# Kernel optimization log

Measured on AMD Instinct MI355X. Metric: run time of the kernel, lower is better.

Reference implementation:

```python
import jax, jax.numpy as jnp
import numpy as np

N, B, T = 2048, 16, 256

def setup_inputs() -> dict:
    key = jax.random.key(0)
    k1, k2, k3, k4 = jax.random.split(key, 4)
    x = jax.random.normal(k1, (B, T, N), dtype=jnp.float32)
    weight = jax.random.normal(k2, (T, T), dtype=jnp.float32) * (1.0 / np.sqrt(T))
    bias = jax.random.normal(k3, (T,), dtype=jnp.float32) * 0.01
    # Gumbel(0,1) noise, matching torch.nn.functional.gumbel_softmax internals
    u = jax.random.uniform(k4, (N * N, 2), dtype=jnp.float32, minval=1e-6, maxval=1.0 - 1e-6)
    gumbel = -jnp.log(-jnp.log(u))
    return {"x": x, "weight": weight, "bias": bias, "gumbel": gumbel}

def reference(x, weight, bias, gumbel):
    # x: [B, T, N] -> node-major [N, B, T]
    xp = jnp.transpose(x, (2, 0, 1))
    n = xp.shape[0]
    # --- similarity-based logits (torch writes via .data -> no grad path) ---
    xs = jax.lax.stop_gradient(xp)
    x_avg = xs.mean(axis=1)                                          # [N, T]
    x_norm = x_avg / jnp.maximum(jnp.linalg.norm(x_avg, axis=-1, keepdims=True), 1e-12)
    sim = (x_norm @ x_norm.T + 1.0) * 0.5                            # [N, N] in [0,1]
    sim_flat = sim.reshape(-1)
    # gumbel_softmax(hard=True) forward: adjacency = argmax over (logits + g)
    score0 = sim_flat + gumbel[:, 0]
    score1 = (1.0 - sim_flat) + gumbel[:, 1]
    adj = (score0 > score1).astype(xp.dtype).reshape(n, n)           # directed adjacency
    # --- structural coefficient (dense, faithful to compute_structural_coeff) ---
    adj_sym = jnp.clip(adj + adj.T, 0.0, 1.0)
    nmask = jnp.clip(adj_sym + jnp.eye(n, dtype=xp.dtype), 0.0, 1.0)
    common = nmask @ nmask.T                                         # common-neighbor counts
    max_common = common.max()                                        # >= 1 (diagonal)
    valid = (adj_sym * (common > 1.0).astype(xp.dtype)) > 0
    struct = jnp.where(valid, (common / max_common) * common, 0.0)   # lambda_val = 1.0
    # edge weights only at directed-edge positions
    W = adj * struct                                                 # [src, dst]
    # --- gcn_norm (no self loops, improved=False): deg over dst, D^-1/2 W D^-1/2 ---
    deg = W.sum(axis=0)
    dinv = jnp.where(deg > 0, deg ** -0.5, 0.0)
    Wn = dinv[:, None] * W * dinv[None, :]
    # --- linear + gather-multiply-scatter aggregation (out[d] = sum_s Wn[s,d] x[s]) ---
    xw = jnp.einsum('nbt,to->nbo', xp, weight)                       # [N, B, T]
    out = jnp.einsum('sd,sbt->dbt', Wn, xw) + bias                   # [N, B, T]
    return jnp.transpose(out, (1, 2, 0))                             # [B, T, N]
```

## Files before the change

kernel.cpp:

```cpp
#include <hip/hip_runtime.h>

#define NN 2048
#define BB 16
#define TT 256

typedef unsigned short ushort_t;
typedef unsigned char u8;
typedef short bf16x8 __attribute__((ext_vector_type(8)));
typedef float f32x4 __attribute__((ext_vector_type(4)));
typedef int i32x4 __attribute__((ext_vector_type(4)));

__device__ __forceinline__ ushort_t f2bf(float f) {
    unsigned u = __float_as_uint(f);
    return (ushort_t)((u + 0x7FFFu + ((u >> 16) & 1u)) >> 16);
}

__device__ __forceinline__ void gload16(const void* g, void* l) {
    __builtin_amdgcn_global_load_lds((const __attribute__((address_space(1))) unsigned int*)g,
                                     (__attribute__((address_space(3))) unsigned int*)l,
                                     16, 0, 0);
}

__device__ __forceinline__ void loop_bf16_128x64(
    const ushort_t* __restrict__ Ag, size_t lda,
    const ushort_t* __restrict__ Bg, size_t ldb,
    int m0, int n0, int nkt,
    ushort_t (*As)[128][32], ushort_t (*Bs)[64][32],
    f32x4 (&acc)[4][2], int tid)
{
    const int lane = tid & 63, wave = tid >> 6;
    const int wr = wave >> 1, wc = wave & 1;
    const int r0 = tid >> 2, kc = (tid & 3) * 8;
    const int lr = lane & 15, kg = (lane >> 4) * 8;
    gload16(&Ag[(size_t)(m0 + r0) * lda + kc], &As[0][r0][kc]);
    gload16(&Ag[(size_t)(m0 + r0 + 64) * lda + kc], &As[0][r0 + 64][kc]);
    gload16(&Bg[(size_t)(n0 + r0) * ldb + kc], &Bs[0][r0][kc]);
    __syncthreads();
    int cur = 0;
    for (int kt = 0; kt < nkt; kt++) {
        if (kt + 1 < nkt) {
            const int k0 = (kt + 1) * 32;
            gload16(&Ag[(size_t)(m0 + r0) * lda + k0 + kc], &As[cur ^ 1][r0][kc]);
            gload16(&Ag[(size_t)(m0 + r0 + 64) * lda + k0 + kc], &As[cur ^ 1][r0 + 64][kc]);
            gload16(&Bg[(size_t)(n0 + r0) * ldb + k0 + kc], &Bs[cur ^ 1][r0][kc]);
        }
        bf16x8 af[4], bfj[2];
#pragma unroll
        for (int f = 0; f < 4; f++) af[f] = *(const bf16x8*)&As[cur][wr * 64 + f * 16 + lr][kg];
#pragma unroll
        for (int j = 0; j < 2; j++) bfj[j] = *(const bf16x8*)&Bs[cur][wc * 32 + j * 16 + lr][kg];
#pragma unroll
        for (int i = 0; i < 4; i++)
#pragma unroll
            for (int j = 0; j < 2; j++)
                acc[i][j] = __builtin_amdgcn_mfma_f32_16x16x32_bf16(af[i], bfj[j], acc[i][j], 0, 0, 0);
        __syncthreads();
        cur ^= 1;
    }
}

__device__ __forceinline__ void loop_i8_128x64(
    const u8* __restrict__ Ag, size_t lda,
    const u8* __restrict__ Bg, size_t ldb,
    int m0, int n0, int nkt,
    u8 (*As)[128][64], u8 (*Bs)[64][64],
    i32x4 (&acc)[4][2], int tid)
{
    const int lane = tid & 63, wave = tid >> 6;
    const int wr = wave >> 1, wc = wave & 1;
    const int r0 = tid >> 2, kc = (tid & 3) * 16;
    const int lr = lane & 15, kg = (lane >> 4) * 16;
    gload16(&Ag[(size_t)(m0 + r0) * lda + kc], &As[0][r0][kc]);
    gload16(&Ag[(size_t)(m0 + r0 + 64) * lda + kc], &As[0][r0 + 64][kc]);
    gload16(&Bg[(size_t)(n0 + r0) * ldb + kc], &Bs[0][r0][kc]);
    __syncthreads();
    int cur = 0;
    for (int kt = 0; kt < nkt; kt++) {
        if (kt + 1 < nkt) {
            const int k0 = (kt + 1) * 64;
            gload16(&Ag[(size_t)(m0 + r0) * lda + k0 + kc], &As[cur ^ 1][r0][kc]);
            gload16(&Ag[(size_t)(m0 + r0 + 64) * lda + k0 + kc], &As[cur ^ 1][r0 + 64][kc]);
            gload16(&Bg[(size_t)(n0 + r0) * ldb + k0 + kc], &Bs[cur ^ 1][r0][kc]);
        }
        i32x4 af[4], bfj[2];
#pragma unroll
        for (int f = 0; f < 4; f++) af[f] = *(const i32x4*)&As[cur][wr * 64 + f * 16 + lr][kg];
#pragma unroll
        for (int j = 0; j < 2; j++) bfj[j] = *(const i32x4*)&Bs[cur][wc * 32 + j * 16 + lr][kg];
#pragma unroll
        for (int i = 0; i < 4; i++)
#pragma unroll
            for (int j = 0; j < 2; j++)
                acc[i][j] = __builtin_amdgcn_mfma_i32_16x16x64_i8(af[i], bfj[j], acc[i][j], 0, 0, 0);
        __syncthreads();
        cur ^= 1;
    }
}

__global__ __launch_bounds__(256) void k_xts(const float* __restrict__ x,
                                             ushort_t* __restrict__ xT,
                                             float* __restrict__ xsumT,
                                             float* __restrict__ ssq) {
    __shared__ float tile[32][33];
    __shared__ float ssqp[32];
    const int n0 = blockIdx.x * 32, t0 = blockIdx.y * 32;
    const int tid = threadIdx.x;
    const int r = tid >> 3, c4 = (tid & 7) * 4;
    if (tid < 32) ssqp[tid] = 0.f;
    float4 acc = {0.f, 0.f, 0.f, 0.f};
    for (int b = 0; b < BB; b++) {
        const float4 v = *(const float4*)&x[(size_t)((b * TT) + t0 + r) * NN + n0 + c4];
        acc.x += v.x; acc.y += v.y; acc.z += v.z; acc.w += v.w;
        __syncthreads();
        tile[r][c4 + 0] = v.x; tile[r][c4 + 1] = v.y;
        tile[r][c4 + 2] = v.z; tile[r][c4 + 3] = v.w;
        __syncthreads();
        ushort4 o;
        o.x = f2bf(tile[c4 + 0][r]); o.y = f2bf(tile[c4 + 1][r]);
        o.z = f2bf(tile[c4 + 2][r]); o.w = f2bf(tile[c4 + 3][r]);
        *(ushort4*)&xT[(size_t)(b * NN + n0 + r) * TT + t0 + c4] = o;
    }
    *(float4*)&xsumT[(size_t)(t0 + r) * NN + n0 + c4] = acc;
    atomicAdd(&ssqp[c4 + 0], acc.x * acc.x);
    atomicAdd(&ssqp[c4 + 1], acc.y * acc.y);
    atomicAdd(&ssqp[c4 + 2], acc.z * acc.z);
    atomicAdd(&ssqp[c4 + 3], acc.w * acc.w);
    __syncthreads();
    if (tid < 32) atomicAdd(&ssq[n0 + tid], ssqp[tid]);
}

__global__ __launch_bounds__(256) void k_adj(const float* __restrict__ A,
                                             const float* __restrict__ ssq,
                                             const float* __restrict__ gumbel,
                                             u8* __restrict__ adjb) {
    __shared__ __align__(16) float As[2][32][64];
    __shared__ __align__(16) float Bs[2][32][64];
    const int m0 = blockIdx.y * 64, n0 = blockIdx.x * 64;
    const int tid = threadIdx.x;
    const int tx = tid & 15, ty = tid >> 4;
    const int sr = tid >> 4, sc = (tid & 15) * 4;
    float acc[4][4];
#pragma unroll
    for (int i = 0; i < 4; i++)
#pragma unroll
        for (int j = 0; j < 4; j++) acc[i][j] = 0.f;
    gload16(&A[(size_t)sr * NN + m0 + sc], &As[0][sr][sc]);
    gload16(&A[(size_t)sr * NN + n0 + sc], &Bs[0][sr][sc]);
    gload16(&A[(size_t)(sr + 16) * NN + m0 + sc], &As[0][sr + 16][sc]);
    gload16(&A[(size_t)(sr + 16) * NN + n0 + sc], &Bs[0][sr + 16][sc]);
    __syncthreads();
    int cur = 0;
    for (int kt = 0; kt < 8; kt++) {
        if (kt + 1 < 8) {
            const int k0 = (kt + 1) * 32;
            gload16(&A[(size_t)(k0 + sr) * NN + m0 + sc], &As[cur ^ 1][sr][sc]);
            gload16(&A[(size_t)(k0 + sr) * NN + n0 + sc], &Bs[cur ^ 1][sr][sc]);
            gload16(&A[(size_t)(k0 + sr + 16) * NN + m0 + sc], &As[cur ^ 1][sr + 16][sc]);
            gload16(&A[(size_t)(k0 + sr + 16) * NN + n0 + sc], &Bs[cur ^ 1][sr + 16][sc]);
        }
#pragma unroll 16
        for (int kk = 0; kk < 32; kk++) {
            float4 a = *(const float4*)&As[cur][kk][ty * 4];
            float4 b = *(const float4*)&Bs[cur][kk][tx * 4];
            const float av[4] = {a.x, a.y, a.z, a.w};
            const float bv[4] = {b.x, b.y, b.z, b.w};
#pragma unroll
            for (int i = 0; i < 4; i++)
#pragma unroll
                for (int j = 0; j < 4; j++) acc[i][j] = fmaf(av[i], bv[j], acc[i][j]);
        }
        __syncthreads();
        cur ^= 1;
    }
    float invi[4], invj[4];
#pragma unroll
    for (int i = 0; i < 4; i++) {
        const float si = ssq[m0 + ty * 4 + i];
        invi[i] = (si > 0.f) ? rsqrtf(si) : 0.f;
        const float sj = ssq[n0 + tx * 4 + i];
        invj[i] = (sj > 0.f) ? rsqrtf(sj) : 0.f;
    }
#pragma unroll
    for (int i = 0; i < 4; i++) {
        const int gi = m0 + ty * 4 + i;
        const size_t rowb = (size_t)gi * NN + n0 + tx * 4;
#pragma unroll
        for (int j = 0; j < 4; j++) {
            const float dot = acc[i][j] * invi[i] * invj[j];
            const float2 g = *(const float2*)&gumbel[2 * (rowb + j)];
            adjb[rowb + j] = (dot > g.y - g.x) ? (u8)1 : (u8)0;
        }
    }
}

__global__ __launch_bounds__(256) void k_nmask(const u8* __restrict__ adjb,
                                               u8* __restrict__ nm) {
    __shared__ u8 tt[32][33];
    const int J = blockIdx.x * 32, I = blockIdx.y * 32;
    const int c = threadIdx.x & 31, r0 = threadIdx.x >> 5;
#pragma unroll
    for (int r = r0; r < 32; r += 8) tt[r][c] = adjb[(size_t)(J + r) * NN + I + c];
    __syncthreads();
#pragma unroll
    for (int r = r0; r < 32; r += 8) {
        const int gi = I + r, gj = J + c;
        const bool on = (gi == gj) || adjb[(size_t)gi * NN + gj] || tt[c][r];
        nm[(size_t)gi * NN + gj] = on ? (u8)1 : (u8)0;
    }
}

__global__ __launch_bounds__(256) void k_commonW(const u8* __restrict__ nm,
                                                 const u8* __restrict__ adjb,
                                                 float* __restrict__ W,
                                                 float* __restrict__ deg) {
    __shared__ __align__(16) u8 As[2][128][64];
    __shared__ __align__(16) u8 Bs[2][64][64];
    const int m0 = blockIdx.y * 128, n0 = blockIdx.x * 64;
    const int tid = threadIdx.x;
    const int lane = tid & 63, wave = tid >> 6;
    const int wr = wave >> 1, wc = wave & 1;
    i32x4 acc[4][2];
#pragma unroll
    for (int i = 0; i < 4; i++)
#pragma unroll
        for (int j = 0; j < 2; j++) acc[i][j] = (i32x4){0, 0, 0, 0};
    loop_i8_128x64(nm, NN, nm, NN, m0, n0, NN / 64, As, Bs, acc, tid);
    const int lr = lane & 15, rg = (lane >> 4) * 4;
#pragma unroll
    for (int j = 0; j < 2; j++) {
        const int gj = n0 + wc * 32 + j * 16 + lr;
        float psum = 0.f;
#pragma unroll
        for (int i = 0; i < 4; i++)
#pragma unroll
            for (int r = 0; r < 4; r++) {
                const int gi = m0 + wr * 64 + i * 16 + rg + r;
                const int cv = acc[i][j][r];
                const size_t fl = (size_t)gi * NN + gj;
                const float cf = (float)cv;
                const float wv = (cv > 1 && adjb[fl]) ? cf * cf : 0.f;
                W[fl] = wv;
                psum += wv;
            }
        atomicAdd(&deg[gj], psum);
    }
}

__global__ __launch_bounds__(256) void k_wtn(const float* __restrict__ W,
                                             const float* __restrict__ deg,
                                             ushort_t* __restrict__ Wtn) {
    __shared__ float tt[64][65];
    const int S0 = blockIdx.x * 64, D0 = blockIdx.y * 64;
    const int c = threadIdx.x & 63, r0 = threadIdx.x >> 6;
#pragma unroll
    for (int r = r0; r < 64; r += 4) tt[r][c] = W[(size_t)(S0 + r) * NN + D0 + c];
    __syncthreads();
    const float dgs = deg[S0 + c];
    const float ds = (dgs > 0.f) ? rsqrtf(dgs) : 0.f;
#pragma unroll
    for (int r = r0; r < 64; r += 4) {
        const int d = D0 + r;
        const float dgd = deg[d];
        const float dd = (dgd > 0.f) ? rsqrtf(dgd) : 0.f;
        Wtn[(size_t)d * NN + S0 + c] = f2bf(tt[c][r] * ds * dd);
    }
}

__global__ __launch_bounds__(256) void k_wt(const float* __restrict__ w,
                                            ushort_t* __restrict__ wT) {
    __shared__ float tile[64][65];
    const int t0 = blockIdx.y * 64, o0 = blockIdx.x * 64;
    const int c = threadIdx.x & 63, r0 = threadIdx.x >> 6;
#pragma unroll
    for (int r = r0; r < 64; r += 4)
        tile[r][c] = w[(size_t)(t0 + r) * TT + o0 + c];
    __syncthreads();
#pragma unroll
    for (int r = r0; r < 64; r += 4)
        wT[(size_t)(o0 + r) * TT + t0 + c] = f2bf(tile[c][r]);
}

__global__ __launch_bounds__(256) void k_xw(const ushort_t* __restrict__ wT,
                                            const ushort_t* __restrict__ xT,
                                            ushort_t* __restrict__ xwT) {
    __shared__ __align__(16) ushort_t As[2][128][32];
    __shared__ __align__(16) ushort_t Bs[2][64][32];
    const int b = blockIdx.z;
    const ushort_t* __restrict__ Bg = xT + (size_t)b * NN * TT;
    const int m0 = blockIdx.y * 128, n0 = blockIdx.x * 64;
    const int tid = threadIdx.x;
    const int lane = tid & 63, wave = tid >> 6;
    const int wr = wave >> 1, wc = wave & 1;
    f32x4 acc[4][2];
#pragma unroll
    for (int i = 0; i < 4; i++)
#pragma unroll
        for (int j = 0; j < 2; j++) acc[i][j] = (f32x4){0.f, 0.f, 0.f, 0.f};
    loop_bf16_128x64(wT, TT, Bg, TT, m0, n0, TT / 32, As, Bs, acc, tid);
    const int lr = lane & 15, rg = (lane >> 4) * 4;
#pragma unroll
    for (int i = 0; i < 4; i++)
#pragma unroll
        for (int j = 0; j < 2; j++)
#pragma unroll
            for (int r = 0; r < 4; r++) {
                const int o = m0 + wr * 64 + i * 16 + rg + r;
                const int n = n0 + wc * 32 + j * 16 + lr;
                xwT[((size_t)b * TT + o) * NN + n] = f2bf(acc[i][j][r]);
            }
}

__global__ __launch_bounds__(256) void k_out(const ushort_t* __restrict__ xwT,
                                             const ushort_t* __restrict__ Wtn,
                                             const float* __restrict__ bias,
                                             float* __restrict__ out) {
    __shared__ __align__(16) ushort_t As[2][128][32];
    __shared__ __align__(16) ushort_t Bs[2][64][32];
    const int m0 = blockIdx.y * 128, n0 = blockIdx.x * 64;
    const int tid = threadIdx.x;
    const int lane = tid & 63, wave = tid >> 6;
    const int wr = wave >> 1, wc = wave & 1;
    f32x4 acc[4][2];
#pragma unroll
    for (int i = 0; i < 4; i++)
#pragma unroll
        for (int j = 0; j < 2; j++) acc[i][j] = (f32x4){0.f, 0.f, 0.f, 0.f};
    loop_bf16_128x64(xwT, NN, Wtn, NN, m0, n0, NN / 32, As, Bs, acc, tid);
    const int lr = lane & 15, rg = (lane >> 4) * 4;
#pragma unroll
    for (int i = 0; i < 4; i++)
#pragma unroll
        for (int j = 0; j < 2; j++)
#pragma unroll
            for (int r = 0; r < 4; r++) {
                const int gm = m0 + wr * 64 + i * 16 + rg + r;
                const int gd = n0 + wc * 32 + j * 16 + lr;
                out[(size_t)gm * NN + gd] = acc[i][j][r] + bias[gm & (TT - 1)];
            }
}

extern "C" void kernel_launch(void* const* d_in, const int* in_sizes, int n_in,
                              void* d_out, int out_size, void* d_ws, size_t ws_size,
                              hipStream_t stream) {
    const float* x      = (const float*)d_in[0];
    const float* w      = (const float*)d_in[1];
    const float* bias   = (const float*)d_in[2];
    const float* gumbel = (const float*)d_in[3];
    float* out = (float*)d_out;

    char* ws = (char*)d_ws;
    float*    xsumT = (float*)(ws + 0);
    float*    ssq   = (float*)(ws + 2097152);
    float*    deg   = (float*)(ws + 2105344);
    u8*       adjb  = (u8*)(ws + 2113536);
    u8*       nm    = (u8*)(ws + 6307840);
    float*    W     = (float*)(ws + 10502144);
    ushort_t* xwT   = (ushort_t*)(ws + 10502144);
    ushort_t* Wtn   = (ushort_t*)(ws + 27279360);
    ushort_t* xT    = (ushort_t*)(ws + 35667968);
    ushort_t* wT    = (ushort_t*)(ws + 52445184);

    hipMemsetAsync(ws + 2097152, 0, 16384, stream);

    k_xts    <<<dim3(NN / 32, TT / 32), 256, 0, stream>>>(x, xT, xsumT, ssq);
    k_adj    <<<dim3(32, 32),           256, 0, stream>>>(xsumT, ssq, gumbel, adjb);
    k_nmask  <<<dim3(64, 64),           256, 0, stream>>>(adjb, nm);
    k_commonW<<<dim3(NN / 64, NN / 128),256, 0, stream>>>(nm, adjb, W, deg);
    k_wtn    <<<dim3(32, 32),           256, 0, stream>>>(W, deg, Wtn);
    k_wt     <<<dim3(4, 4),             256, 0, stream>>>(w, wT);
    k_xw     <<<dim3(NN / 64, TT / 128, BB), 256, 0, stream>>>(wT, xT, xwT);
    k_out    <<<dim3(NN / 64, (BB * TT) / 128), 256, 0, stream>>>(xwT, Wtn, bias, out);
}
```

Baseline: 281.3 us.

## Triple-buffer GEMM mainloops with one barrier and enlarge bf16 tiles to 128x128

Replaces the double-buffered GEMM loops with a three-stage LDS ring. Loads are issued two tiles ahead and retired with explicit vmcnt waits and a single s_barrier per k-step instead of two __syncthreads. The bf16 GEMMs (xw and out) also grow from 128x64 to 128x128 block tiles with 4x4 MFMA accumulators per wave, improving operand reuse and halving the grid. The cost is more LDS and registers per block and fewer blocks on the GPU, which may lower occupancy and wave-level parallelism.

```diff
diff --git a/kernel.cpp b/kernel.cpp
--- a/kernel.cpp
+++ b/kernel.cpp
@@ -21,45 +21,50 @@
                                      16, 0, 0);
 }
 
-__device__ __forceinline__ void loop_bf16_128x64(
+#define SBAR() asm volatile("s_barrier" ::: "memory")
+
+__device__ __forceinline__ void mfma3_bf16_128(
     const ushort_t* __restrict__ Ag, size_t lda,
     const ushort_t* __restrict__ Bg, size_t ldb,
     int m0, int n0, int nkt,
-    ushort_t (*As)[128][32], ushort_t (*Bs)[64][32],
-    f32x4 (&acc)[4][2], int tid)
+    ushort_t (*As)[128][32], ushort_t (*Bs)[128][32],
+    f32x4 (&acc)[4][4], int tid)
 {
     const int lane = tid & 63, wave = tid >> 6;
     const int wr = wave >> 1, wc = wave & 1;
     const int r0 = tid >> 2, kc = (tid & 3) * 8;
     const int lr = lane & 15, kg = (lane >> 4) * 8;
-    gload16(&Ag[(size_t)(m0 + r0) * lda + kc], &As[0][r0][kc]);
-    gload16(&Ag[(size_t)(m0 + r0 + 64) * lda + kc], &As[0][r0 + 64][kc]);
-    gload16(&Bg[(size_t)(n0 + r0) * ldb + kc], &Bs[0][r0][kc]);
-    __syncthreads();
-    int cur = 0;
+#define STAGE_BF(kt, buf) { \
+        const int k0_ = (kt) * 32; \
+        gload16(&Ag[(size_t)(m0 + r0) * lda + k0_ + kc], &As[buf][r0][kc]); \
+        gload16(&Ag[(size_t)(m0 + r0 + 64) * lda + k0_ + kc], &As[buf][r0 + 64][kc]); \
+        gload16(&Bg[(size_t)(n0 + r0) * ldb + k0_ + kc], &Bs[buf][r0][kc]); \
+        gload16(&Bg[(size_t)(n0 + r0 + 64) * ldb + k0_ + kc], &Bs[buf][r0 + 64][kc]); \
+    }
+    STAGE_BF(0, 0);
+    STAGE_BF(1, 1);
     for (int kt = 0; kt < nkt; kt++) {
-        if (kt + 1 < nkt) {
-            const int k0 = (kt + 1) * 32;
-            gload16(&Ag[(size_t)(m0 + r0) * lda + k0 + kc], &As[cur ^ 1][r0][kc]);
-            gload16(&Ag[(size_t)(m0 + r0 + 64) * lda + k0 + kc], &As[cur ^ 1][r0 + 64][kc]);
-            gload16(&Bg[(size_t)(n0 + r0) * ldb + k0 + kc], &Bs[cur ^ 1][r0][kc]);
+        if (kt + 1 < nkt) asm volatile("s_waitcnt vmcnt(4)" ::: "memory");
+        else              asm volatile("s_waitcnt vmcnt(0)" ::: "memory");
+        SBAR();
+        if (kt + 2 < nkt) STAGE_BF(kt + 2, (kt + 2) % 3);
+        const int cur = kt % 3;
+        bf16x8 af[4], bfj[4];
+#pragma unroll
+        for (int f = 0; f < 4; f++) {
+            af[f]  = *(const bf16x8*)&As[cur][wr * 64 + f * 16 + lr][kg];
+            bfj[f] = *(const bf16x8*)&Bs[cur][wc * 64 + f * 16 + lr][kg];
         }
-        bf16x8 af[4], bfj[2];
-#pragma unroll
-        for (int f = 0; f < 4; f++) af[f] = *(const bf16x8*)&As[cur][wr * 64 + f * 16 + lr][kg];
-#pragma unroll
-        for (int j = 0; j < 2; j++) bfj[j] = *(const bf16x8*)&Bs[cur][wc * 32 + j * 16 + lr][kg];
 #pragma unroll
         for (int i = 0; i < 4; i++)
 #pragma unroll
-            for (int j = 0; j < 2; j++)
+            for (int j = 0; j < 4; j++)
                 acc[i][j] = __builtin_amdgcn_mfma_f32_16x16x32_bf16(af[i], bfj[j], acc[i][j], 0, 0, 0);
-        __syncthreads();
-        cur ^= 1;
-    }
-}
-
-__device__ __forceinline__ void loop_i8_128x64(
+    }
+#undef STAGE_BF
+}
+
+__device__ __forceinline__ void mfma3_i8_128x64(
     const u8* __restrict__ Ag, size_t lda,
     const u8* __restrict__ Bg, size_t ldb,
     int m0, int n0, int nkt,
@@ -70,18 +75,20 @@
     const int wr = wave >> 1, wc = wave & 1;
     const int r0 = tid >> 2, kc = (tid & 3) * 16;
     const int lr = lane & 15, kg = (lane >> 4) * 16;
-    gload16(&Ag[(size_t)(m0 + r0) * lda + kc], &As[0][r0][kc]);
-    gload16(&Ag[(size_t)(m0 + r0 + 64) * lda + kc], &As[0][r0 + 64][kc]);
-    gload16(&Bg[(size_t)(n0 + r0) * ldb + kc], &Bs[0][r0][kc]);
-    __syncthreads();
-    int cur = 0;
+#define STAGE_I8(kt, buf) { \
+        const int k0_ = (kt) * 64; \
+        gload16(&Ag[(size_t)(m0 + r0) * lda + k0_ + kc], &As[buf][r0][kc]); \
+        gload16(&Ag[(size_t)(m0 + r0 + 64) * lda + k0_ + kc], &As[buf][r0 + 64][kc]); \
+        gload16(&Bg[(size_t)(n0 + r0) * ldb + k0_ + kc], &Bs[buf][r0][kc]); \
+    }
+    STAGE_I8(0, 0);
+    STAGE_I8(1, 1);
     for (int kt = 0; kt < nkt; kt++) {
-        if (kt + 1 < nkt) {
-            const int k0 = (kt + 1) * 64;
-            gload16(&Ag[(size_t)(m0 + r0) * lda + k0 + kc], &As[cur ^ 1][r0][kc]);
-            gload16(&Ag[(size_t)(m0 + r0 + 64) * lda + k0 + kc], &As[cur ^ 1][r0 + 64][kc]);
-            gload16(&Bg[(size_t)(n0 + r0) * ldb + k0 + kc], &Bs[cur ^ 1][r0][kc]);
-        }
+        if (kt + 1 < nkt) asm volatile("s_waitcnt vmcnt(3)" ::: "memory");
+        else              asm volatile("s_waitcnt vmcnt(0)" ::: "memory");
+        SBAR();
+        if (kt + 2 < nkt) STAGE_I8(kt + 2, (kt + 2) % 3);
+        const int cur = kt % 3;
         i32x4 af[4], bfj[2];
 #pragma unroll
         for (int f = 0; f < 4; f++) af[f] = *(const i32x4*)&As[cur][wr * 64 + f * 16 + lr][kg];
@@ -92,9 +99,8 @@
 #pragma unroll
             for (int j = 0; j < 2; j++)
                 acc[i][j] = __builtin_amdgcn_mfma_i32_16x16x64_i8(af[i], bfj[j], acc[i][j], 0, 0, 0);
-        __syncthreads();
-        cur ^= 1;
-    }
+    }
+#undef STAGE_I8
 }
 
 __global__ __launch_bounds__(256) void k_xts(const float* __restrict__ x,
@@ -213,8 +219,8 @@
                                                  const u8* __restrict__ adjb,
                                                  float* __restrict__ W,
                                                  float* __restrict__ deg) {
-    __shared__ __align__(16) u8 As[2][128][64];
-    __shared__ __align__(16) u8 Bs[2][64][64];
+    __shared__ __align__(16) u8 As[3][128][64];
+    __shared__ __align__(16) u8 Bs[3][64][64];
     const int m0 = blockIdx.y * 128, n0 = blockIdx.x * 64;
     const int tid = threadIdx.x;
     const int lane = tid & 63, wave = tid >> 6;
@@ -224,7 +230,7 @@
     for (int i = 0; i < 4; i++)
 #pragma unroll
         for (int j = 0; j < 2; j++) acc[i][j] = (i32x4){0, 0, 0, 0};
-    loop_i8_128x64(nm, NN, nm, NN, m0, n0, NN / 64, As, Bs, acc, tid);
+    mfma3_i8_128x64(nm, NN, nm, NN, m0, n0, NN / 64, As, Bs, acc, tid);
     const int lr = lane & 15, rg = (lane >> 4) * 4;
 #pragma unroll
     for (int j = 0; j < 2; j++) {
@@ -283,29 +289,29 @@
 __global__ __launch_bounds__(256) void k_xw(const ushort_t* __restrict__ wT,
                                             const ushort_t* __restrict__ xT,
                                             ushort_t* __restrict__ xwT) {
-    __shared__ __align__(16) ushort_t As[2][128][32];
-    __shared__ __align__(16) ushort_t Bs[2][64][32];
+    __shared__ __align__(16) ushort_t As[3][128][32];
+    __shared__ __align__(16) ushort_t Bs[3][128][32];
     const int b = blockIdx.z;
     const ushort_t* __restrict__ Bg = xT + (size_t)b * NN * TT;
-    const int m0 = blockIdx.y * 128, n0 = blockIdx.x * 64;
-    const int tid = threadIdx.x;
-    const int lane = tid & 63, wave = tid >> 6;
-    const int wr = wave >> 1, wc = wave & 1;
-    f32x4 acc[4][2];
-#pragma unroll
-    for (int i = 0; i < 4; i++)
-#pragma unroll
-        for (int j = 0; j < 2; j++) acc[i][j] = (f32x4){0.f, 0.f, 0.f, 0.f};
-    loop_bf16_128x64(wT, TT, Bg, TT, m0, n0, TT / 32, As, Bs, acc, tid);
+    const int m0 = blockIdx.y * 128, n0 = blockIdx.x * 128;
+    const int tid = threadIdx.x;
+    const int lane = tid & 63, wave = tid >> 6;
+    const int wr = wave >> 1, wc = wave & 1;
+    f32x4 acc[4][4];
+#pragma unroll
+    for (int i = 0; i < 4; i++)
+#pragma unroll
+        for (int j = 0; j < 4; j++) acc[i][j] = (f32x4){0.f, 0.f, 0.f, 0.f};
+    mfma3_bf16_128(wT, TT, Bg, TT, m0, n0, TT / 32, As, Bs, acc, tid);
     const int lr = lane & 15, rg = (lane >> 4) * 4;
 #pragma unroll
     for (int i = 0; i < 4; i++)
 #pragma unroll
-        for (int j = 0; j < 2; j++)
+        for (int j = 0; j < 4; j++)
 #pragma unroll
             for (int r = 0; r < 4; r++) {
                 const int o = m0 + wr * 64 + i * 16 + rg + r;
-                const int n = n0 + wc * 32 + j * 16 + lr;
+                const int n = n0 + wc * 64 + j * 16 + lr;
                 xwT[((size_t)b * TT + o) * NN + n] = f2bf(acc[i][j][r]);
             }
 }
@@ -314,27 +320,27 @@
                                              const ushort_t* __restrict__ Wtn,
                                              const float* __restrict__ bias,
                                              float* __restrict__ out) {
-    __shared__ __align__(16) ushort_t As[2][128][32];
-    __shared__ __align__(16) ushort_t Bs[2][64][32];
-    const int m0 = blockIdx.y * 128, n0 = blockIdx.x * 64;
-    const int tid = threadIdx.x;
-    const int lane = tid & 63, wave = tid >> 6;
-    const int wr = wave >> 1, wc = wave & 1;
-    f32x4 acc[4][2];
-#pragma unroll
-    for (int i = 0; i < 4; i++)
-#pragma unroll
-        for (int j = 0; j < 2; j++) acc[i][j] = (f32x4){0.f, 0.f, 0.f, 0.f};
-    loop_bf16_128x64(xwT, NN, Wtn, NN, m0, n0, NN / 32, As, Bs, acc, tid);
+    __shared__ __align__(16) ushort_t As[3][128][32];
+    __shared__ __align__(16) ushort_t Bs[3][128][32];
+    const int m0 = blockIdx.y * 128, n0 = blockIdx.x * 128;
+    const int tid = threadIdx.x;
+    const int lane = tid & 63, wave = tid >> 6;
+    const int wr = wave >> 1, wc = wave & 1;
+    f32x4 acc[4][4];
+#pragma unroll
+    for (int i = 0; i < 4; i++)
+#pragma unroll
+        for (int j = 0; j < 4; j++) acc[i][j] = (f32x4){0.f, 0.f, 0.f, 0.f};
+    mfma3_bf16_128(xwT, NN, Wtn, NN, m0, n0, NN / 32, As, Bs, acc, tid);
     const int lr = lane & 15, rg = (lane >> 4) * 4;
 #pragma unroll
     for (int i = 0; i < 4; i++)
 #pragma unroll
-        for (int j = 0; j < 2; j++)
+        for (int j = 0; j < 4; j++)
 #pragma unroll
             for (int r = 0; r < 4; r++) {
                 const int gm = m0 + wr * 64 + i * 16 + rg + r;
-                const int gd = n0 + wc * 32 + j * 16 + lr;
+                const int gd = n0 + wc * 64 + j * 16 + lr;
                 out[(size_t)gm * NN + gd] = acc[i][j][r] + bias[gm & (TT - 1)];
             }
 }
@@ -368,6 +374,6 @@
     k_commonW<<<dim3(NN / 64, NN / 128),256, 0, stream>>>(nm, adjb, W, deg);
     k_wtn    <<<dim3(32, 32),           256, 0, stream>>>(W, deg, Wtn);
     k_wt     <<<dim3(4, 4),             256, 0, stream>>>(w, wT);
-    k_xw     <<<dim3(NN / 64, TT / 128, BB), 256, 0, stream>>>(wT, xT, xwT);
-    k_out    <<<dim3(NN / 64, (BB * TT) / 128), 256, 0, stream>>>(xwT, Wtn, bias, out);
-}
+    k_xw     <<<dim3(NN / 128, TT / 128, BB),   256, 0, stream>>>(wT, xT, xwT);
+    k_out    <<<dim3(NN / 128, (BB * TT) / 128), 256, 0, stream>>>(xwT, Wtn, bias, out);
+}
```

New measurement: 275.6 us. 1.02x faster.
